# Kernel tuning notes

Hardware: AMD Instinct MI355X
Metric: run time of the kernel (lower is better)

The kernel has to match this reference:

```python
import jax, jax.numpy as jnp
import numpy as np


def setup_inputs() -> dict:
    key = jax.random.key(0)
    k1, k2 = jax.random.split(key)
    b, n, d = 4, 4096, 1024
    x = jax.random.normal(k1, (b, n, d), dtype=jnp.float32)
    t = jax.random.normal(k2, (2 * n, d), dtype=jnp.float32)
    return {"x": x, "t": t}


def reference(x, t):
    # x: (b, n, d); t: (2*l, d) with l = max(n, m); m = n here.
    n = x.shape[1]
    m = n
    l = max(n, m)
    L = 2 * l
    x_fft = jnp.fft.rfft(x, n=L, axis=-2)            # (b, L//2+1, d) complex
    t_fft = jnp.fft.rfft(t[None, :, :], n=L, axis=-2)  # (1, L//2+1, d)
    o = jnp.fft.irfft(x_fft * t_fft, n=L, axis=-2)   # (b, L, d)
    return o[:, :m]
```

## Files before the change

kernel.cpp:

```cpp
#include <hip/hip_runtime.h>
#include <hip/hip_bf16.h>

#define NFFT 8192
#define NH   4096
#define D    1024
#define NSEQ 4096
#define NDP  512
#define BATCH 4
#define NT   512
#define PI_D 3.14159265358979323846

#define C1 0.92387953251128675613f
#define S1 0.38268343236508977173f
#define RT 0.70710678118654752440f

__device__ __forceinline__ int SWZ(int i) { return i ^ ((i >> 4) & 15) ^ ((i >> 8) & 15); }

__device__ __forceinline__ float2 cadd(float2 a, float2 b){ return make_float2(a.x+b.x, a.y+b.y); }
__device__ __forceinline__ float2 csub(float2 a, float2 b){ return make_float2(a.x-b.x, a.y-b.y); }
__device__ __forceinline__ float2 cmul(float2 a, float2 w){ return make_float2(a.x*w.x - a.y*w.y, a.x*w.y + a.y*w.x); }
__device__ __forceinline__ float2 cmulc(float2 a, float2 w){ return make_float2(a.x*w.x + a.y*w.y, a.y*w.x - a.x*w.y); }

__device__ __forceinline__ int drev16(int k) {
    return ((k & 1) << 12) | (((k >> 1) & 15) << 8) | (((k >> 5) & 15) << 4) | ((k >> 9) & 15);
}
__device__ __forceinline__ int kmap16(int tid, int it) {
    return ((tid >> 7) & 3) | (it << 2) | ((tid & 15) << 5) | (((tid >> 4) & 7) << 9);
}
__device__ __forceinline__ int drev12(int k) {
    return ((k & 15) << 8) | (((k >> 4) & 15) << 4) | ((k >> 8) & 15);
}

__global__ __launch_bounds__(256) void wtab_init(float2* __restrict__ wtab) {
    int m = blockIdx.x * 256 + threadIdx.x;
    double a = -2.0 * PI_D * (double)m / (double)NFFT;
    wtab[m] = make_float2((float)cos(a), (float)sin(a));
}

template<bool INV>
__device__ __forceinline__ void dft16(float2 v[16]) {
    float2 s[4][4];
    #pragma unroll
    for (int i = 0; i < 4; ++i) {
        float2 z0=v[i], z1=v[i+4], z2=v[i+8], z3=v[i+12];
        float2 A=cadd(z0,z2), Cc=csub(z0,z2), B=cadd(z1,z3), Dd=csub(z1,z3);
        s[i][0] = cadd(A,B);
        s[i][2] = csub(A,B);
        if (!INV) { s[i][1] = make_float2(Cc.x+Dd.y, Cc.y-Dd.x);
                    s[i][3] = make_float2(Cc.x-Dd.y, Cc.y+Dd.x); }
        else      { s[i][1] = make_float2(Cc.x-Dd.y, Cc.y+Dd.x);
                    s[i][3] = make_float2(Cc.x+Dd.y, Cc.y-Dd.x); }
    }
    if (!INV) {
        s[1][1]=cmul(s[1][1],make_float2(C1,-S1)); s[1][2]=cmul(s[1][2],make_float2(RT,-RT)); s[1][3]=cmul(s[1][3],make_float2(S1,-C1));
        s[2][1]=cmul(s[2][1],make_float2(RT,-RT)); s[2][2]=make_float2(s[2][2].y,-s[2][2].x); s[2][3]=cmul(s[2][3],make_float2(-RT,-RT));
        s[3][1]=cmul(s[3][1],make_float2(S1,-C1)); s[3][2]=cmul(s[3][2],make_float2(-RT,-RT)); s[3][3]=cmul(s[3][3],make_float2(-C1,S1));
    } else {
        s[1][1]=cmul(s[1][1],make_float2(C1,S1));  s[1][2]=cmul(s[1][2],make_float2(RT,RT));  s[1][3]=cmul(s[1][3],make_float2(S1,C1));
        s[2][1]=cmul(s[2][1],make_float2(RT,RT));  s[2][2]=make_float2(-s[2][2].y,s[2][2].x); s[2][3]=cmul(s[2][3],make_float2(-RT,RT));
        s[3][1]=cmul(s[3][1],make_float2(S1,C1));  s[3][2]=cmul(s[3][2],make_float2(-RT,RT)); s[3][3]=cmul(s[3][3],make_float2(-C1,-S1));
    }
    #pragma unroll
    for (int o = 0; o < 4; ++o) {
        float2 z0=s[0][o], z1=s[1][o], z2=s[2][o], z3=s[3][o];
        float2 A=cadd(z0,z2), Cc=csub(z0,z2), B=cadd(z1,z3), Dd=csub(z1,z3);
        v[o]    = cadd(A,B);
        v[o+8]  = csub(A,B);
        if (!INV) { v[o+4]  = make_float2(Cc.x+Dd.y, Cc.y-Dd.x);
                    v[o+12] = make_float2(Cc.x-Dd.y, Cc.y+Dd.x); }
        else      { v[o+4]  = make_float2(Cc.x-Dd.y, Cc.y+Dd.x);
                    v[o+12] = make_float2(Cc.x+Dd.y, Cc.y-Dd.x); }
    }
}

__device__ __forceinline__ void twiddle_fwd(float2 v[16], const float2* __restrict__ wt, int tw1i) {
    float2 w1 = wt[tw1i];
    float2 w2 = cmul(w1,w1), w3 = cmul(w2,w1), w4 = cmul(w2,w2), w8 = cmul(w4,w4), w12 = cmul(w8,w4);
    v[1]=cmul(v[1],w1);  v[2]=cmul(v[2],w2);  v[3]=cmul(v[3],w3);
    v[4]=cmul(v[4],w4);  v[5]=cmul(v[5],cmul(w4,w1));  v[6]=cmul(v[6],cmul(w4,w2));  v[7]=cmul(v[7],cmul(w4,w3));
    v[8]=cmul(v[8],w8);  v[9]=cmul(v[9],cmul(w8,w1));  v[10]=cmul(v[10],cmul(w8,w2)); v[11]=cmul(v[11],cmul(w8,w3));
    v[12]=cmul(v[12],w12); v[13]=cmul(v[13],cmul(w12,w1)); v[14]=cmul(v[14],cmul(w12,w2)); v[15]=cmul(v[15],cmul(w12,w3));
}
__device__ __forceinline__ void twiddle_inv(float2 v[16], const float2* __restrict__ wt, int tw1i) {
    float2 w1 = wt[tw1i];
    float2 w2 = cmul(w1,w1), w3 = cmul(w2,w1), w4 = cmul(w2,w2), w8 = cmul(w4,w4), w12 = cmul(w8,w4);
    v[1]=cmulc(v[1],w1);  v[2]=cmulc(v[2],w2);  v[3]=cmulc(v[3],w3);
    v[4]=cmulc(v[4],w4);  v[5]=cmulc(v[5],cmul(w4,w1));  v[6]=cmulc(v[6],cmul(w4,w2));  v[7]=cmulc(v[7],cmul(w4,w3));
    v[8]=cmulc(v[8],w8);  v[9]=cmulc(v[9],cmul(w8,w1));  v[10]=cmulc(v[10],cmul(w8,w2)); v[11]=cmulc(v[11],cmul(w8,w3));
    v[12]=cmulc(v[12],w12); v[13]=cmulc(v[13],cmul(w12,w1)); v[14]=cmulc(v[14],cmul(w12,w2)); v[15]=cmulc(v[15],cmul(w12,w3));
}

template<int H, bool TW, bool INV>
__device__ __forceinline__ void pass16(float2* zs, const float2* __restrict__ wt, int t) {
    int blk = t >> 8;
    int i0, tw1i;
    if (H == 256)      { int j = t & 255;                      i0 = blk*4096 + j;           tw1i = 2*j;  }
    else if (H == 16)  { int g = (t>>4) & 15; int j = t & 15;  i0 = blk*4096 + g*256 + j;   tw1i = 32*j; }
    else               { int g = t & 255;                      i0 = blk*4096 + g*16;        tw1i = 0;    }
    float2 v[16];
    #pragma unroll
    for (int q = 0; q < 16; ++q) v[q] = zs[SWZ(i0 + H*q)];
    if (INV && TW) twiddle_inv(v, wt, tw1i);
    dft16<INV>(v);
    if (!INV && TW) twiddle_fwd(v, wt, tw1i);
    #pragma unroll
    for (int r = 0; r < 16; ++r) zs[SWZ(i0 + H*r)] = v[r];
}

template<int H, bool TW, bool INV>
__device__ __forceinline__ void pass16q(float2* zs, const float2* __restrict__ wt, int t) {
    int i0, tw1i;
    if (H == 16) { int g = t >> 4, j = t & 15; i0 = g*256 + j; tw1i = 32*j; }
    else         { i0 = t*16; tw1i = 0; }
    float2 v[16];
    #pragma unroll
    for (int q = 0; q < 16; ++q) v[q] = zs[SWZ(i0 + H*q)];
    if (INV && TW) twiddle_inv(v, wt, tw1i);
    dft16<INV>(v);
    if (!INV && TW) twiddle_fwd(v, wt, tw1i);
    #pragma unroll
    for (int r = 0; r < 16; ++r) zs[SWZ(i0 + H*r)] = v[r];
}

__global__ __launch_bounds__(NT, 2) void tspec_kernel(const float* __restrict__ tg,
                                                      const float2* __restrict__ wt,
                                                      float4* __restrict__ tsPall) {
    __shared__ float2 zs[NFFT];
    int wg = blockIdx.x;
    int dp = ((wg & 7) << 6) | (wg >> 3);
    int t  = threadIdx.x;

    const float* tb = tg + 2 * dp;
    #pragma unroll
    for (int it = 0; it < 8; ++it) {
        int idx = t + it * NT;
        float2 v0 = *(const float2*)(tb + (size_t)idx * D);
        float2 v1 = *(const float2*)(tb + (size_t)(idx + NH) * D);
        zs[SWZ(idx)]      = cadd(v0, v1);
        zs[SWZ(idx + NH)] = cmul(csub(v0, v1), wt[idx]);
    }
    __syncthreads();
    pass16<256, true,  false>(zs, wt, t); __syncthreads();
    pass16<16,  true,  false>(zs, wt, t); __syncthreads();
    pass16<1,   false, false>(zs, wt, t); __syncthreads();

    #pragma unroll
    for (int it = 0; it < 8; ++it) {
        int k  = kmap16(t, it);
        int p1 = drev16(k);
        int p2 = drev16((NFFT - k) & (NFFT - 1));
        float2 z1 = zs[SWZ(p1)], z2 = zs[SWZ(p2)];
        float2 T0 = make_float2(0.5f*(z1.x + z2.x), 0.5f*(z1.y - z2.y));
        float2 T1 = make_float2(0.5f*(z1.y + z2.y), 0.5f*(z2.x - z1.x));
        int s   = (k <= 2048) ? k : (4096 - k);
        int lin = (s == 2048) ? 2048
                              : ((s & 7) * 256 + (((s >> 8) & 7) | (((s >> 3) & 31) << 3)));
        float2* w0 = (float2*)(tsPall + ((size_t)(2*dp)     * 2049 + lin));
        float2* w1 = (float2*)(tsPall + ((size_t)(2*dp + 1) * 2049 + lin));
        if (k < 2048)      { w0[0] = T0; w1[0] = T1; }
        else if (k > 2048) { w0[1] = T0; w1[1] = T1; }
        else               { w0[0] = T0; w0[1] = T0; w1[0] = T1; w1[1] = T1; }
    }
    if (t == 0) {
        float2 zn = zs[SWZ(8)];
        float2* w0 = (float2*)(tsPall + (size_t)(2*dp)     * 2049);
        float2* w1 = (float2*)(tsPall + (size_t)(2*dp + 1) * 2049);
        w0[1] = make_float2(zn.x, 0.f);
        w1[1] = make_float2(zn.y, 0.f);
    }
}

__device__ __forceinline__ void conv_pair(float2* zs, const float2* __restrict__ wt,
                                          float4 Tq, int k) {
    int p1 = drev12(k);
    int kp = (4096 - k) & 4095;
    int p2 = drev12(kp);
    float2 Zk = zs[SWZ(p1)], Zp = zs[SWZ(p2)];
    float2 w = wt[k];
    float Ar = 0.5f*(Zk.x + Zp.x), Ai = 0.5f*(Zk.y - Zp.y);
    float Br = 0.5f*(Zk.y + Zp.y), Bi = 0.5f*(Zp.x - Zk.x);
    float2 WB = make_float2(w.x*Br - w.y*Bi, w.x*Bi + w.y*Br);
    float2 X1 = make_float2(Ar + WB.x, Ai + WB.y);
    float2 X2 = make_float2(Ar - WB.x, WB.y - Ai);
    float2 Y1 = make_float2(X1.x*Tq.x - X1.y*Tq.y, X1.x*Tq.y + X1.y*Tq.x);
    float2 Y2 = make_float2(X2.x*Tq.z - X2.y*Tq.w, X2.x*Tq.w + X2.y*Tq.z);
    float Er = 0.5f*(Y1.x + Y2.x), Ei = 0.5f*(Y1.y - Y2.y);
    float Gr = 0.5f*(Y1.x - Y2.x), Gi = 0.5f*(Y1.y + Y2.y);
    float O1x = Gr*w.x + Gi*w.y, O1y = Gi*w.x - Gr*w.y;
    float O2x = O1x,             O2y = Gr*w.y - Gi*w.x;
    zs[SWZ(p1)] = make_float2(Er - O1y, Ei + O1x);
    zs[SWZ(p2)] = make_float2(Er - O2y, O2x - Ei);
}

template<int PACKED>
__global__ __launch_bounds__(256, 2) void conv_kernel(float* __restrict__ region,
                                                      const float* __restrict__ xg,
                                                      float* __restrict__ outg,
                                                      const float2* __restrict__ wt,
                                                      const float4* __restrict__ tsPall) {
    __shared__ float2 zs[4096];
    int wg  = blockIdx.x;
    int c   = (wg & 7) * 128 + ((wg >> 3) & 127);
    int b   = wg >> 10;
    int t   = threadIdx.x;

    float* slab = PACKED ? (region + ((size_t)c * BATCH + b) * NSEQ) : nullptr;

    {
        float2 v[16];
        #pragma unroll
        for (int q = 0; q < 8; ++q) {
            int n = t + 256*q;
            if (PACKED) v[q] = *(const float2*)(slab + 2*n);
            else {
                const float* xb = xg + (size_t)b * NSEQ * D + c;
                v[q] = make_float2(xb[(size_t)(2*n) * D], xb[(size_t)(2*n+1) * D]);
            }
        }
        #pragma unroll
        for (int q = 8; q < 16; ++q) v[q] = make_float2(0.f, 0.f);
        dft16<false>(v);
        twiddle_fwd(v, wt, 2*t);
        #pragma unroll
        for (int r = 0; r < 16; ++r) zs[SWZ(t + 256*r)] = v[r];
    }
    __syncthreads();
    pass16q<16, true,  false>(zs, wt, t); __syncthreads();
    pass16q<1,  false, false>(zs, wt, t); __syncthreads();

    const float4* tsP = tsPall + (size_t)c * 2049;
    #pragma unroll
    for (int it = 0; it < 8; ++it) {
        int k = ((t & 7) << 8) | ((t >> 3) << 3) | it;
        conv_pair(zs, wt, tsP[it * 256 + t], k);
    }
    if (t == 0) conv_pair(zs, wt, tsP[2048], 2048);
    __syncthreads();

    pass16q<1,  false, true>(zs, wt, t); __syncthreads();
    pass16q<16, true,  true>(zs, wt, t); __syncthreads();

    {
        float2 v[16];
        #pragma unroll
        for (int q = 0; q < 16; ++q) v[q] = zs[SWZ(t + 256*q)];
        twiddle_inv(v, wt, 2*t);
        dft16<true>(v);
        const float sc = 1.0f / 4096.0f;
        #pragma unroll
        for (int r = 0; r < 8; ++r) {
            int n = t + 256*r;
            float2 rv = make_float2(v[r].x * sc, v[r].y * sc);
            if (PACKED) *(float2*)(slab + 2*n) = rv;
            else {
                float* ob = outg + (size_t)b * NSEQ * D + c;
                ob[(size_t)(2*n) * D]   = rv.x;
                ob[(size_t)(2*n+1) * D] = rv.y;
            }
        }
    }
}

__global__ __launch_bounds__(256) void pack_xQ(const float* __restrict__ in,
                                               float* __restrict__ q) {
    __shared__ float tile[64][65];
    int tid = threadIdx.x;
    int n0 = blockIdx.x * 64, d0 = blockIdx.y * 64, b = blockIdx.z;
    const float* ib = in + (size_t)b * NSEQ * D;
    #pragma unroll
    for (int it = 0; it < 16; ++it) {
        int n_l = it * 4 + (tid >> 6);
        int d_l = tid & 63;
        tile[n_l][d_l] = ib[(size_t)(n0 + n_l) * D + d0 + d_l];
    }
    __syncthreads();
    #pragma unroll
    for (int it = 0; it < 16; ++it) {
        int flat = it * 256 + tid;
        int c_l = flat >> 6;
        int n_l = flat & 63;
        q[((size_t)(d0 + c_l) * BATCH + b) * NSEQ + n0 + n_l] = tile[n_l][c_l];
    }
}

__global__ __launch_bounds__(256) void unpack_Q(const float* __restrict__ q,
                                                float* __restrict__ outp) {
    __shared__ float tile[64][65];
    int tid = threadIdx.x;
    int n0 = blockIdx.x * 64, d0 = blockIdx.y * 64, b = blockIdx.z;
    #pragma unroll
    for (int it = 0; it < 16; ++it) {
        int flat = it * 256 + tid;
        int c_l = flat >> 6;
        int n_l = flat & 63;
        tile[c_l][n_l] = q[((size_t)(d0 + c_l) * BATCH + b) * NSEQ + n0 + n_l];
    }
    __syncthreads();
    float* ob = outp + (size_t)b * NSEQ * D;
    #pragma unroll
    for (int it = 0; it < 16; ++it) {
        int n_l = it * 4 + (tid >> 6);
        int d_l = tid & 63;
        ob[(size_t)(n0 + n_l) * D + d0 + d_l] = tile[d_l][n_l];
    }
}

extern "C" void kernel_launch(void* const* d_in, const int* in_sizes, int n_in,
                              void* d_out, int out_size, void* d_ws, size_t ws_size,
                              hipStream_t stream) {
    const float* x = (const float*)d_in[0];
    const float* t = (const float*)d_in[1];
    float* outp = (float*)d_out;

    char* ws = (char*)d_ws;
    float2* wtab  = (float2*)ws;
    float4* tsPall = (float4*)(ws + 65536);
    const size_t OFF_Q = 65536 + (size_t)1024 * 2049 * 16;
    float* region = (float*)(ws + OFF_Q);
    const size_t need_full = OFF_Q + (size_t)1024 * BATCH * NSEQ * sizeof(float);

    wtab_init<<<16, 256, 0, stream>>>(wtab);
    tspec_kernel<<<NDP, NT, 0, stream>>>(t, wtab, tsPall);

    if (ws_size >= need_full) {
        pack_xQ<<<dim3(64, 16, BATCH), 256, 0, stream>>>(x, region);
        conv_kernel<1><<<1024 * BATCH, 256, 0, stream>>>(region, nullptr, nullptr, wtab, tsPall);
        unpack_Q<<<dim3(64, 16, BATCH), 256, 0, stream>>>(region, outp);
    } else {
        conv_kernel<0><<<1024 * BATCH, 256, 0, stream>>>(nullptr, x, outp, wtab, tsPall);
    }
}
```

Measured before the change: 156.7 us.

## Drop unpack pass and recompute t spectrum with per-channel half-size real FFT

The conv kernel now writes its outputs straight to the strided output layout, so the separate unpack transpose kernel and its round trip through the workspace go away. The t-spectrum kernel is restructured to process one channel per block with a 4096-point complex FFT on even/odd packed samples, in place of a two-channels-per-block 8192-point FFT. This halves shared memory per block and doubles the block count. The trade-off is strided, uncoalesced column writes in the conv epilogue and strided scalar loads of t.

```diff
diff --git a/kernel.cpp b/kernel.cpp
--- a/kernel.cpp
+++ b/kernel.cpp
@@ -5,9 +5,7 @@
 #define NH   4096
 #define D    1024
 #define NSEQ 4096
-#define NDP  512
 #define BATCH 4
-#define NT   512
 #define PI_D 3.14159265358979323846
 
 #define C1 0.92387953251128675613f
@@ -21,12 +19,6 @@
 __device__ __forceinline__ float2 cmul(float2 a, float2 w){ return make_float2(a.x*w.x - a.y*w.y, a.x*w.y + a.y*w.x); }
 __device__ __forceinline__ float2 cmulc(float2 a, float2 w){ return make_float2(a.x*w.x + a.y*w.y, a.y*w.x - a.x*w.y); }
 
-__device__ __forceinline__ int drev16(int k) {
-    return ((k & 1) << 12) | (((k >> 1) & 15) << 8) | (((k >> 5) & 15) << 4) | ((k >> 9) & 15);
-}
-__device__ __forceinline__ int kmap16(int tid, int it) {
-    return ((tid >> 7) & 3) | (it << 2) | ((tid & 15) << 5) | (((tid >> 4) & 7) << 9);
-}
 __device__ __forceinline__ int drev12(int k) {
     return ((k & 15) << 8) | (((k >> 4) & 15) << 4) | ((k >> 8) & 15);
 }
@@ -91,23 +83,6 @@
 }
 
 template<int H, bool TW, bool INV>
-__device__ __forceinline__ void pass16(float2* zs, const float2* __restrict__ wt, int t) {
-    int blk = t >> 8;
-    int i0, tw1i;
-    if (H == 256)      { int j = t & 255;                      i0 = blk*4096 + j;           tw1i = 2*j;  }
-    else if (H == 16)  { int g = (t>>4) & 15; int j = t & 15;  i0 = blk*4096 + g*256 + j;   tw1i = 32*j; }
-    else               { int g = t & 255;                      i0 = blk*4096 + g*16;        tw1i = 0;    }
-    float2 v[16];
-    #pragma unroll
-    for (int q = 0; q < 16; ++q) v[q] = zs[SWZ(i0 + H*q)];
-    if (INV && TW) twiddle_inv(v, wt, tw1i);
-    dft16<INV>(v);
-    if (!INV && TW) twiddle_fwd(v, wt, tw1i);
-    #pragma unroll
-    for (int r = 0; r < 16; ++r) zs[SWZ(i0 + H*r)] = v[r];
-}
-
-template<int H, bool TW, bool INV>
 __device__ __forceinline__ void pass16q(float2* zs, const float2* __restrict__ wt, int t) {
     int i0, tw1i;
     if (H == 16) { int g = t >> 4, j = t & 15; i0 = g*256 + j; tw1i = 32*j; }
@@ -122,51 +97,47 @@
     for (int r = 0; r < 16; ++r) zs[SWZ(i0 + H*r)] = v[r];
 }
 
-__global__ __launch_bounds__(NT, 2) void tspec_kernel(const float* __restrict__ tg,
-                                                      const float2* __restrict__ wt,
-                                                      float4* __restrict__ tsPall) {
-    __shared__ float2 zs[NFFT];
+__global__ __launch_bounds__(256, 2) void tspec_kernel(const float* __restrict__ tg,
+                                                       const float2* __restrict__ wt,
+                                                       float4* __restrict__ tsPall) {
+    __shared__ float2 zs[4096];
     int wg = blockIdx.x;
-    int dp = ((wg & 7) << 6) | (wg >> 3);
+    int c  = (wg & 7) * 128 + (wg >> 3);
     int t  = threadIdx.x;
 
-    const float* tb = tg + 2 * dp;
+    const float* tb = tg + c;
+    {
+        float2 v[16];
+        #pragma unroll
+        for (int q = 0; q < 16; ++q) {
+            int n = t + 256*q;
+            v[q] = make_float2(tb[(size_t)(2*n) * D], tb[(size_t)(2*n+1) * D]);
+        }
+        dft16<false>(v);
+        twiddle_fwd(v, wt, 2*t);
+        #pragma unroll
+        for (int r = 0; r < 16; ++r) zs[SWZ(t + 256*r)] = v[r];
+    }
+    __syncthreads();
+    pass16q<16, true,  false>(zs, wt, t); __syncthreads();
+    pass16q<1,  false, false>(zs, wt, t); __syncthreads();
+
+    float4* o = tsPall + (size_t)c * 2049;
     #pragma unroll
     for (int it = 0; it < 8; ++it) {
-        int idx = t + it * NT;
-        float2 v0 = *(const float2*)(tb + (size_t)idx * D);
-        float2 v1 = *(const float2*)(tb + (size_t)(idx + NH) * D);
-        zs[SWZ(idx)]      = cadd(v0, v1);
-        zs[SWZ(idx + NH)] = cmul(csub(v0, v1), wt[idx]);
-    }
-    __syncthreads();
-    pass16<256, true,  false>(zs, wt, t); __syncthreads();
-    pass16<16,  true,  false>(zs, wt, t); __syncthreads();
-    pass16<1,   false, false>(zs, wt, t); __syncthreads();
-
-    #pragma unroll
-    for (int it = 0; it < 8; ++it) {
-        int k  = kmap16(t, it);
-        int p1 = drev16(k);
-        int p2 = drev16((NFFT - k) & (NFFT - 1));
-        float2 z1 = zs[SWZ(p1)], z2 = zs[SWZ(p2)];
-        float2 T0 = make_float2(0.5f*(z1.x + z2.x), 0.5f*(z1.y - z2.y));
-        float2 T1 = make_float2(0.5f*(z1.y + z2.y), 0.5f*(z2.x - z1.x));
-        int s   = (k <= 2048) ? k : (4096 - k);
-        int lin = (s == 2048) ? 2048
-                              : ((s & 7) * 256 + (((s >> 8) & 7) | (((s >> 3) & 31) << 3)));
-        float2* w0 = (float2*)(tsPall + ((size_t)(2*dp)     * 2049 + lin));
-        float2* w1 = (float2*)(tsPall + ((size_t)(2*dp + 1) * 2049 + lin));
-        if (k < 2048)      { w0[0] = T0; w1[0] = T1; }
-        else if (k > 2048) { w0[1] = T0; w1[1] = T1; }
-        else               { w0[0] = T0; w0[1] = T0; w1[0] = T1; w1[1] = T1; }
+        int k  = ((t & 7) << 8) | ((t >> 3) << 3) | it;
+        int p1 = drev12(k);
+        int p2 = drev12((4096 - k) & 4095);
+        float2 Zk = zs[SWZ(p1)], Zp = zs[SWZ(p2)];
+        float Er = 0.5f*(Zk.x + Zp.x), Ei = 0.5f*(Zk.y - Zp.y);
+        float Or = 0.5f*(Zk.y + Zp.y), Oi = 0.5f*(Zp.x - Zk.x);
+        float2 w = wt[k];
+        float WOr = Or*w.x - Oi*w.y, WOi = Or*w.y + Oi*w.x;
+        o[it * 256 + t] = make_float4(Er + WOr, Ei + WOi, Er - WOr, WOi - Ei);
     }
     if (t == 0) {
-        float2 zn = zs[SWZ(8)];
-        float2* w0 = (float2*)(tsPall + (size_t)(2*dp)     * 2049);
-        float2* w1 = (float2*)(tsPall + (size_t)(2*dp + 1) * 2049);
-        w0[1] = make_float2(zn.x, 0.f);
-        w1[1] = make_float2(zn.y, 0.f);
+        float2 Zk = zs[SWZ(drev12(2048))];
+        o[2048] = make_float4(Zk.x, -Zk.y, Zk.x, -Zk.y);
     }
 }
 
@@ -193,7 +164,7 @@
 }
 
 template<int PACKED>
-__global__ __launch_bounds__(256, 2) void conv_kernel(float* __restrict__ region,
+__global__ __launch_bounds__(256, 2) void conv_kernel(const float* __restrict__ region,
                                                       const float* __restrict__ xg,
                                                       float* __restrict__ outg,
                                                       const float2* __restrict__ wt,
@@ -204,16 +175,17 @@
     int b   = wg >> 10;
     int t   = threadIdx.x;
 
-    float* slab = PACKED ? (region + ((size_t)c * BATCH + b) * NSEQ) : nullptr;
-
     {
         float2 v[16];
-        #pragma unroll
-        for (int q = 0; q < 8; ++q) {
-            int n = t + 256*q;
-            if (PACKED) v[q] = *(const float2*)(slab + 2*n);
-            else {
-                const float* xb = xg + (size_t)b * NSEQ * D + c;
+        if (PACKED) {
+            const float* slab = region + ((size_t)c * BATCH + b) * NSEQ;
+            #pragma unroll
+            for (int q = 0; q < 8; ++q) v[q] = *(const float2*)(slab + 2*(t + 256*q));
+        } else {
+            const float* xb = xg + (size_t)b * NSEQ * D + c;
+            #pragma unroll
+            for (int q = 0; q < 8; ++q) {
+                int n = t + 256*q;
                 v[q] = make_float2(xb[(size_t)(2*n) * D], xb[(size_t)(2*n+1) * D]);
             }
         }
@@ -247,16 +219,12 @@
         twiddle_inv(v, wt, 2*t);
         dft16<true>(v);
         const float sc = 1.0f / 4096.0f;
+        float* ob = outg + (size_t)b * NSEQ * D + c;
         #pragma unroll
         for (int r = 0; r < 8; ++r) {
             int n = t + 256*r;
-            float2 rv = make_float2(v[r].x * sc, v[r].y * sc);
-            if (PACKED) *(float2*)(slab + 2*n) = rv;
-            else {
-                float* ob = outg + (size_t)b * NSEQ * D + c;
-                ob[(size_t)(2*n) * D]   = rv.x;
-                ob[(size_t)(2*n+1) * D] = rv.y;
-            }
+            ob[(size_t)(2*n) * D]   = v[r].x * sc;
+            ob[(size_t)(2*n+1) * D] = v[r].y * sc;
         }
     }
 }
@@ -283,28 +251,6 @@
     }
 }
 
-__global__ __launch_bounds__(256) void unpack_Q(const float* __restrict__ q,
-                                                float* __restrict__ outp) {
-    __shared__ float tile[64][65];
-    int tid = threadIdx.x;
-    int n0 = blockIdx.x * 64, d0 = blockIdx.y * 64, b = blockIdx.z;
-    #pragma unroll
-    for (int it = 0; it < 16; ++it) {
-        int flat = it * 256 + tid;
-        int c_l = flat >> 6;
-        int n_l = flat & 63;
-        tile[c_l][n_l] = q[((size_t)(d0 + c_l) * BATCH + b) * NSEQ + n0 + n_l];
-    }
-    __syncthreads();
-    float* ob = outp + (size_t)b * NSEQ * D;
-    #pragma unroll
-    for (int it = 0; it < 16; ++it) {
-        int n_l = it * 4 + (tid >> 6);
-        int d_l = tid & 63;
-        ob[(size_t)(n0 + n_l) * D + d0 + d_l] = tile[d_l][n_l];
-    }
-}
-
 extern "C" void kernel_launch(void* const* d_in, const int* in_sizes, int n_in,
                               void* d_out, int out_size, void* d_ws, size_t ws_size,
                               hipStream_t stream) {
@@ -313,19 +259,18 @@
     float* outp = (float*)d_out;
 
     char* ws = (char*)d_ws;
-    float2* wtab  = (float2*)ws;
+    float2* wtab   = (float2*)ws;
     float4* tsPall = (float4*)(ws + 65536);
     const size_t OFF_Q = 65536 + (size_t)1024 * 2049 * 16;
     float* region = (float*)(ws + OFF_Q);
     const size_t need_full = OFF_Q + (size_t)1024 * BATCH * NSEQ * sizeof(float);
 
     wtab_init<<<16, 256, 0, stream>>>(wtab);
-    tspec_kernel<<<NDP, NT, 0, stream>>>(t, wtab, tsPall);
+    tspec_kernel<<<1024, 256, 0, stream>>>(t, wtab, tsPall);
 
     if (ws_size >= need_full) {
         pack_xQ<<<dim3(64, 16, BATCH), 256, 0, stream>>>(x, region);
-        conv_kernel<1><<<1024 * BATCH, 256, 0, stream>>>(region, nullptr, nullptr, wtab, tsPall);
-        unpack_Q<<<dim3(64, 16, BATCH), 256, 0, stream>>>(region, outp);
+        conv_kernel<1><<<1024 * BATCH, 256, 0, stream>>>(region, nullptr, outp, wtab, tsPall);
     } else {
         conv_kernel<0><<<1024 * BATCH, 256, 0, stream>>>(nullptr, x, outp, wtab, tsPall);
     }
```

After: 193.9 us. 23.7% more time.
